# Performance work log

Measured on AMD Instinct MI355X. Metric: run time of the kernel, lower is better.

Reference implementation:

```python
import jax, jax.numpy as jnp
import numpy as np

H = 2048      # hidden_size
E = 16        # num_experts
I = 512       # moe_intermediate_size
IS = 2048     # shared_expert_intermediate_size
TOP_K = 2
B, S = 1, 2048


def setup_inputs() -> dict:
    key = jax.random.key(0)
    ks = jax.random.split(key, 9)
    std = 0.02
    return {
        "hidden_states": jax.random.normal(ks[0], (B, S, H), dtype=jnp.float32),
        "gate_w": jax.random.normal(ks[1], (E, H), dtype=jnp.float32) * std,
        "w1": jax.random.normal(ks[2], (E, I, H), dtype=jnp.float32) * std,  # gate_proj per expert
        "w2": jax.random.normal(ks[3], (E, H, I), dtype=jnp.float32) * std,  # down_proj per expert
        "w3": jax.random.normal(ks[4], (E, I, H), dtype=jnp.float32) * std,  # up_proj per expert
        "ws_gate": jax.random.normal(ks[5], (IS, H), dtype=jnp.float32) * std,  # shared gate_proj
        "ws_up": jax.random.normal(ks[6], (IS, H), dtype=jnp.float32) * std,    # shared up_proj
        "ws_down": jax.random.normal(ks[7], (H, IS), dtype=jnp.float32) * std,  # shared down_proj
        "shared_gate_w": jax.random.normal(ks[8], (1, H), dtype=jnp.float32) * std,
    }


def reference(hidden_states, gate_w, w1, w2, w3, ws_gate, ws_up, ws_down, shared_gate_w):
    b, s, h = hidden_states.shape
    x = hidden_states.reshape(-1, h)                     # [T, H]
    T = x.shape[0]

    # Router: softmax in fp32, top-k, renormalize (norm_topk_prob=True)
    router_logits = x @ gate_w.T                         # [T, E]
    routing = jax.nn.softmax(router_logits.astype(jnp.float32), axis=-1)
    topw, sel = jax.lax.top_k(routing, TOP_K)            # [T, K]
    topw = topw / jnp.sum(topw, axis=-1, keepdims=True)
    topw = topw.astype(x.dtype)

    # Scatter top-k weights into dense [T, E] combine matrix (torch_moe semantics)
    combine = jnp.zeros((T, E), dtype=x.dtype).at[jnp.arange(T)[:, None], sel].set(topw)

    # Expert SwiGLU MLPs evaluated densely, masked/weighted by combine
    hmid = jax.nn.silu(jnp.einsum('th,eih->tei', x, w1)) * jnp.einsum('th,eih->tei', x, w3)  # [T,E,I]
    hmid = hmid * combine[:, :, None]
    moe_out = jnp.einsum('tei,ehi->th', hmid, w2)        # [T, H]

    # Shared expert with sigmoid gate
    shared = (jax.nn.silu(x @ ws_gate.T) * (x @ ws_up.T)) @ ws_down.T  # [T, H]
    shared = jax.nn.sigmoid(x @ shared_gate_w.T) * shared

    return (moe_out + shared).reshape(b, s, h)
```

## Files before the change

### kernel.cpp

```cpp
#include <hip/hip_runtime.h>
#include <hip/hip_bf16.h>
#include <cmath>

#define HDIM 2048
#define NEXP 16
#define IDIM 512
#define ISDIM 2048
#define NTOK 2048
#define MAXT 48
#define ROWSCAP (MAXT * 128)

#define GU_EXP (MAXT * 4)
#define GU_SH ((NTOK / 128) * (ISDIM / 128))
#define DN_SH ((NTOK / 128) * (HDIM / 256))
#define DN_EXP (MAXT * 8)

typedef short bf16x8 __attribute__((ext_vector_type(8)));
typedef float f32x4 __attribute__((ext_vector_type(4)));
typedef unsigned short us;
typedef __attribute__((address_space(1))) const unsigned int* as1p;
typedef __attribute__((address_space(3))) unsigned int* as3p;

__device__ __forceinline__ us f2bf(float f) {
  unsigned int u = __builtin_bit_cast(unsigned int, f);
  u += 0x7FFFu + ((u >> 16) & 1u);
  return (us)(u >> 16);
}
__device__ __forceinline__ float bf2f(us v) {
  return __builtin_bit_cast(float, (unsigned)v << 16);
}

__device__ __forceinline__ void glds16(const void* g, void* l) {
  __builtin_amdgcn_global_load_lds((as1p)(unsigned long long)g,
                                   (as3p)(unsigned int)(unsigned long long)l, 16, 0, 0);
}

__device__ __forceinline__ void stage_cvt(const float* __restrict__ src,
                                          us* __restrict__ dst) {
  const float4* p = (const float4*)src;
  float4 a = p[0], b = p[1];
  unsigned u0 = __builtin_bit_cast(unsigned, a.x) + 0x8000u;
  unsigned u1 = __builtin_bit_cast(unsigned, a.y) + 0x8000u;
  unsigned u2 = __builtin_bit_cast(unsigned, a.z) + 0x8000u;
  unsigned u3 = __builtin_bit_cast(unsigned, a.w) + 0x8000u;
  unsigned u4 = __builtin_bit_cast(unsigned, b.x) + 0x8000u;
  unsigned u5 = __builtin_bit_cast(unsigned, b.y) + 0x8000u;
  unsigned u6 = __builtin_bit_cast(unsigned, b.z) + 0x8000u;
  unsigned u7 = __builtin_bit_cast(unsigned, b.w) + 0x8000u;
  int4 v;
  v.x = __builtin_amdgcn_perm(u1, u0, 0x07060302);
  v.y = __builtin_amdgcn_perm(u3, u2, 0x07060302);
  v.z = __builtin_amdgcn_perm(u5, u4, 0x07060302);
  v.w = __builtin_amdgcn_perm(u7, u6, 0x07060302);
  *(int4*)dst = v;
}

__global__ __launch_bounds__(256) void k_router(const float* __restrict__ x,
                                                const float* __restrict__ gate_w,
                                                const float* __restrict__ sgw,
                                                us* __restrict__ xb,
                                                int* __restrict__ sel,
                                                float* __restrict__ wnorm,
                                                float* __restrict__ sig,
                                                int* __restrict__ counts) {
  __shared__ float lg[4][17];
  int tid = threadIdx.x, wid = tid >> 6, lane = tid & 63;
  int t = blockIdx.x * 4 + wid;
  const float4* xrow = reinterpret_cast<const float4*>(x + (size_t)t * HDIM);
  float4 xv[8];
#pragma unroll
  for (int s = 0; s < 8; s++) xv[s] = xrow[s * 64 + lane];
  ushort4* xbrow = reinterpret_cast<ushort4*>(xb + (size_t)t * HDIM);
#pragma unroll
  for (int s = 0; s < 8; s++) {
    ushort4 o;
    o.x = f2bf(xv[s].x); o.y = f2bf(xv[s].y); o.z = f2bf(xv[s].z); o.w = f2bf(xv[s].w);
    xbrow[s * 64 + lane] = o;
  }
#pragma unroll 1
  for (int e = 0; e < 17; e++) {
    const float4* gr =
        reinterpret_cast<const float4*>(e < 16 ? gate_w + (size_t)e * HDIM : sgw);
    float acc = 0.f;
#pragma unroll
    for (int s = 0; s < 8; s++) {
      float4 g = gr[s * 64 + lane];
      acc += xv[s].x * g.x + xv[s].y * g.y + xv[s].z * g.z + xv[s].w * g.w;
    }
#pragma unroll
    for (int off = 32; off; off >>= 1) acc += __shfl_xor(acc, off, 64);
    if (lane == 0) lg[wid][e] = acc;
  }
  if (lane == 0) {
    float* L = lg[wid];
    int i1 = 0; float v1 = L[0];
    for (int i = 1; i < NEXP; i++) if (L[i] > v1) { v1 = L[i]; i1 = i; }
    int i2 = (i1 == 0) ? 1 : 0; float v2 = L[i2];
    for (int i = 0; i < NEXP; i++)
      if (i != i1 && i != i2 && L[i] > v2) { v2 = L[i]; i2 = i; }
    float wa = 1.f / (1.f + expf(v2 - v1));
    sel[2 * t] = i1; sel[2 * t + 1] = i2;
    wnorm[2 * t] = wa; wnorm[2 * t + 1] = 1.f - wa;
    sig[t] = 1.f / (1.f + expf(-L[16]));
    atomicAdd(&counts[i1], 1);
    atomicAdd(&counts[i2], 1);
  }
}

__global__ __launch_bounds__(256) void k_scan_scatter(const int* __restrict__ counts,
                                                      const int* __restrict__ sel,
                                                      const float* __restrict__ wnorm,
                                                      int* __restrict__ tile_expert,
                                                      int* __restrict__ row_token,
                                                      int* __restrict__ rowk,
                                                      float* __restrict__ rw) {
  __shared__ int offs_s[NEXP];
  __shared__ int fill_s[NEXP];
  int tid = threadIdx.x;
  for (int r = tid; r < ROWSCAP; r += 256) row_token[r] = -1;
  if (tid < NEXP) fill_s[tid] = 0;
  if (tid == 0) {
    int acc = 0;
    for (int e = 0; e < NEXP; e++) {
      offs_s[e] = acc;
      int nt = (counts[e] + 127) >> 7;
      for (int i = 0; i < nt; i++) tile_expert[(acc >> 7) + i] = e;
      acc += nt << 7;
    }
    for (int m = acc >> 7; m < MAXT; m++) tile_expert[m] = -1;
  }
  __syncthreads();
  for (int t = tid; t < NTOK; t += 256) {
    for (int k = 0; k < 2; k++) {
      int e = sel[2 * t + k];
      int pos = atomicAdd(&fill_s[e], 1);
      int row = offs_s[e] + pos;
      row_token[row] = t;
      rowk[row] = k;
      rw[row] = wnorm[2 * t + k];
    }
  }
}

__global__ __launch_bounds__(512) void k_gu(
    const us* __restrict__ xb, const float* __restrict__ w1,
    const float* __restrict__ w3, const float* __restrict__ wsg,
    const float* __restrict__ wsu, const int* __restrict__ tile_expert,
    const int* __restrict__ row_token, us* __restrict__ hmid,
    us* __restrict__ hs) {
  __shared__ us As[128 * 64];
  __shared__ us Bs[2][128 * 64];
  __shared__ int toks_s[128];
  int bid = blockIdx.x, tid = threadIdx.x;
  int w = tid >> 6, lane = tid & 63;
  const float *bG, *bU;
  us* outp;
  int mt, n0, ostride;
  if (bid < GU_EXP) {
    mt = bid >> 2; int nt = bid & 3;
    int e = tile_expert[mt];
    if (e < 0) return;
    if (tid < 128) {
      int tk = row_token[mt * 128 + tid];
      toks_s[tid] = tk < 0 ? 0 : tk;
    }
    bG = w1 + ((size_t)e * IDIM + nt * 128) * HDIM;
    bU = w3 + ((size_t)e * IDIM + nt * 128) * HDIM;
    outp = hmid; ostride = IDIM; n0 = nt * 128;
  } else {
    int sb = bid - GU_EXP;
    mt = sb >> 4; int nt = sb & 15;
    if (tid < 128) toks_s[tid] = mt * 128 + tid;
    bG = wsg + (size_t)(nt * 128) * HDIM;
    bU = wsu + (size_t)(nt * 128) * HDIM;
    outp = hs; ostride = ISDIM; n0 = nt * 128;
  }
  __syncthreads();
  int lr = lane >> 3, lc = lane & 7;
  int swz = (lc ^ lr) * 8;
  const us* aSrc0 = xb + (size_t)toks_s[w * 16 + lr] * HDIM + swz;
  const us* aSrc1 = xb + (size_t)toks_s[w * 16 + 8 + lr] * HDIM + swz;
  int r0 = tid >> 3, p0 = tid & 7, g0 = p0 ^ (r0 & 7);
  int r1 = (tid + 512) >> 3, g1 = p0 ^ (r1 & 7);
  size_t bo0 = (size_t)r0 * HDIM + g0 * 8;
  size_t bo1 = (size_t)r1 * HDIM + g1 * 8;
  int mat = w >> 2, sub = w & 3, wm = sub >> 1, wn = sub & 1;
  int quad = lane >> 4, l16 = lane & 15, sw = l16 & 7;
  f32x4 acc[4][4] = {};
  for (int k0 = 0; k0 < HDIM; k0 += 64) {
    glds16(aSrc0 + k0, As + w * 1024);
    glds16(aSrc1 + k0, As + w * 1024 + 512);
    stage_cvt(bG + bo0 + k0, &Bs[0][(r0 * 8 + p0) * 8]);
    stage_cvt(bG + bo1 + k0, &Bs[0][(r1 * 8 + p0) * 8]);
    stage_cvt(bU + bo0 + k0, &Bs[1][(r0 * 8 + p0) * 8]);
    stage_cvt(bU + bo1 + k0, &Bs[1][(r1 * 8 + p0) * 8]);
    __syncthreads();
#pragma unroll
    for (int ks = 0; ks < 2; ks++) {
      int cb = (ks * 4 + quad) ^ sw;
      bf16x8 af[4], bf[4];
#pragma unroll
      for (int ms = 0; ms < 4; ms++)
        af[ms] = *(const bf16x8*)&As[((wm * 64 + ms * 16 + l16) * 8 + cb) * 8];
#pragma unroll
      for (int ns = 0; ns < 4; ns++)
        bf[ns] = *(const bf16x8*)&Bs[mat][((wn * 64 + ns * 16 + l16) * 8 + cb) * 8];
#pragma unroll
      for (int ms = 0; ms < 4; ms++)
#pragma unroll
        for (int ns = 0; ns < 4; ns++)
          acc[ms][ns] = __builtin_amdgcn_mfma_f32_16x16x32_bf16(af[ms], bf[ns], acc[ms][ns], 0, 0, 0);
    }
    __syncthreads();
  }
  us* ub = (us*)Bs;
  if (mat == 1) {
#pragma unroll
    for (int ms = 0; ms < 4; ms++)
#pragma unroll
      for (int ns = 0; ns < 4; ns++)
#pragma unroll
        for (int r = 0; r < 4; r++) {
          int row = wm * 64 + ms * 16 + quad * 4 + r;
          int col = wn * 64 + ns * 16 + l16;
          ub[row * 128 + col] = f2bf(acc[ms][ns][r]);
        }
  }
  __syncthreads();
  if (mat == 0) {
#pragma unroll
    for (int ms = 0; ms < 4; ms++)
#pragma unroll
      for (int ns = 0; ns < 4; ns++)
#pragma unroll
        for (int r = 0; r < 4; r++) {
          int row = wm * 64 + ms * 16 + quad * 4 + r;
          int col = wn * 64 + ns * 16 + l16;
          float g = acc[ms][ns][r];
          float u = bf2f(ub[row * 128 + col]);
          float hv = (g / (1.f + __expf(-g))) * u;
          outp[(size_t)(mt * 128 + row) * ostride + n0 + col] = f2bf(hv);
        }
  }
}

__global__ __launch_bounds__(512) void k_down(
    const us* __restrict__ hmid, const us* __restrict__ hs,
    const float* __restrict__ w2, const float* __restrict__ wsd,
    const int* __restrict__ tile_expert, const int* __restrict__ row_token,
    const int* __restrict__ rowk, const float* __restrict__ rw,
    const float* __restrict__ sig, us* __restrict__ slab) {
  __shared__ us As[128 * 64];
  __shared__ us Bs[256 * 64];
  __shared__ int idx_s[128];
  __shared__ float wgt_s[128];
  int bid = blockIdx.x, tid = threadIdx.x;
  int w = tid >> 6, lane = tid & 63;
  const us* aBase;
  const float* bBase;
  int K, mt, n0;
  if (bid < DN_SH) {
    mt = bid >> 3; int nt = bid & 7;
    aBase = hs + (size_t)mt * 128 * ISDIM; K = ISDIM;
    bBase = wsd + (size_t)(nt * 256) * ISDIM;
    n0 = nt * 256;
    if (tid < 128) {
      int t = mt * 128 + tid;
      idx_s[tid] = 2 * NTOK * HDIM + t * HDIM;
      wgt_s[tid] = sig[t];
    }
  } else {
    int sb = bid - DN_SH;
    mt = sb >> 3; int nt = sb & 7;
    int e = tile_expert[mt];
    if (e < 0) return;
    aBase = hmid + (size_t)mt * 128 * IDIM; K = IDIM;
    bBase = w2 + ((size_t)e * HDIM + nt * 256) * IDIM;
    n0 = nt * 256;
    if (tid < 128) {
      int tk = row_token[mt * 128 + tid];
      if (tk < 0) { idx_s[tid] = -1; wgt_s[tid] = 0.f; }
      else {
        idx_s[tid] = (rowk[mt * 128 + tid] * NTOK + tk) * HDIM;
        wgt_s[tid] = rw[mt * 128 + tid];
      }
    }
  }
  __syncthreads();
  int lr = lane >> 3, lc = lane & 7;
  int swz = (lc ^ lr) * 8;
  const us* aSrc0 = aBase + (size_t)(w * 16 + lr) * K + swz;
  const us* aSrc1 = aBase + (size_t)(w * 16 + 8 + lr) * K + swz;
  int r0 = tid >> 3, p0 = tid & 7;
  int wmn = w >> 2, wn = w & 3;
  int quad = lane >> 4, l16 = lane & 15, sw = l16 & 7;
  f32x4 acc[4][4] = {};
  for (int k0 = 0; k0 < K; k0 += 64) {
    glds16(aSrc0 + k0, As + w * 1024);
    glds16(aSrc1 + k0, As + w * 1024 + 512);
#pragma unroll
    for (int j = 0; j < 4; j++) {
      int row = r0 + j * 64;
      int gc = p0 ^ (row & 7);
      stage_cvt(bBase + (size_t)row * K + gc * 8 + k0, &Bs[(row * 8 + p0) * 8]);
    }
    __syncthreads();
#pragma unroll
    for (int ks = 0; ks < 2; ks++) {
      int cb = (ks * 4 + quad) ^ sw;
      bf16x8 af[4], bf[4];
#pragma unroll
      for (int ms = 0; ms < 4; ms++)
        af[ms] = *(const bf16x8*)&As[((wmn * 64 + ms * 16 + l16) * 8 + cb) * 8];
#pragma unroll
      for (int ns = 0; ns < 4; ns++)
        bf[ns] = *(const bf16x8*)&Bs[((wn * 64 + ns * 16 + l16) * 8 + cb) * 8];
#pragma unroll
      for (int ms = 0; ms < 4; ms++)
#pragma unroll
        for (int ns = 0; ns < 4; ns++)
          acc[ms][ns] = __builtin_amdgcn_mfma_f32_16x16x32_bf16(af[ms], bf[ns], acc[ms][ns], 0, 0, 0);
    }
    __syncthreads();
  }
#pragma unroll
  for (int ms = 0; ms < 4; ms++)
#pragma unroll
    for (int r = 0; r < 4; r++) {
      int rr = wmn * 64 + ms * 16 + quad * 4 + r;
      int ix = idx_s[rr];
      if (ix >= 0) {
        float wgt = wgt_s[rr];
        us* orow = slab + (size_t)ix + n0 + wn * 64;
#pragma unroll
        for (int ns = 0; ns < 4; ns++)
          orow[ns * 16 + l16] = f2bf(wgt * acc[ms][ns][r]);
      }
    }
}

__global__ __launch_bounds__(256) void k_combine(const us* __restrict__ slab,
                                                 float* __restrict__ out) {
  size_t i = ((size_t)blockIdx.x * 256 + threadIdx.x) * 8;
  bf16x8 a = *(const bf16x8*)(slab + i);
  bf16x8 b = *(const bf16x8*)(slab + (size_t)NTOK * HDIM + i);
  bf16x8 c = *(const bf16x8*)(slab + 2 * (size_t)NTOK * HDIM + i);
  float4 o[2];
#pragma unroll
  for (int j = 0; j < 8; j++)
    ((float*)o)[j] = bf2f((us)a[j]) + bf2f((us)b[j]) + bf2f((us)c[j]);
  *(float4*)(out + i) = o[0];
  *(float4*)(out + i + 4) = o[1];
}

extern "C" void kernel_launch(void* const* d_in, const int* in_sizes, int n_in,
                              void* d_out, int out_size, void* d_ws, size_t ws_size,
                              hipStream_t stream) {
  const float* x = (const float*)d_in[0];
  const float* gate_w = (const float*)d_in[1];
  const float* w1 = (const float*)d_in[2];
  const float* w2 = (const float*)d_in[3];
  const float* w3 = (const float*)d_in[4];
  const float* wsg = (const float*)d_in[5];
  const float* wsu = (const float*)d_in[6];
  const float* wsd = (const float*)d_in[7];
  const float* sgw = (const float*)d_in[8];
  float* out = (float*)d_out;

  us* xb = (us*)d_ws;
  us* hs = xb + (size_t)NTOK * HDIM;
  us* hmid = hs + (size_t)NTOK * ISDIM;
  us* slab = hmid + (size_t)ROWSCAP * IDIM;
  float* rw = (float*)(slab + (size_t)3 * NTOK * HDIM);
  float* wnorm = rw + ROWSCAP;
  float* sig = wnorm + 2 * NTOK;
  int* sel = (int*)(sig + NTOK);
  int* row_token = sel + 2 * NTOK;
  int* rowk = row_token + ROWSCAP;
  int* counts = rowk + ROWSCAP;
  int* tile_expert = counts + NEXP;

  hipMemsetAsync(counts, 0, NEXP * sizeof(int), stream);
  k_router<<<dim3(NTOK / 4), dim3(256), 0, stream>>>(x, gate_w, sgw, xb, sel, wnorm,
                                                     sig, counts);
  k_scan_scatter<<<dim3(1), dim3(256), 0, stream>>>(counts, sel, wnorm, tile_expert,
                                                    row_token, rowk, rw);
  k_gu<<<dim3(GU_EXP + GU_SH), dim3(512), 0, stream>>>(
      xb, w1, w3, wsg, wsu, tile_expert, row_token, hmid, hs);
  k_down<<<dim3(DN_SH + DN_EXP), dim3(512), 0, stream>>>(
      hmid, hs, w2, wsd, tile_expert, row_token, rowk, rw, sig, slab);
  k_combine<<<dim3(NTOK * HDIM / 2048), dim3(256), 0, stream>>>(slab, out);
}
```

Baseline: 459.5 us.

## Pre-convert weights to bf16 and load GEMM B tiles via direct LDS loads

Adds a kernel that converts all expert and shared weight matrices from fp32 to bf16 into workspace each call. The gate/up and down GEMMs then stage the B operand with asynchronous global-to-LDS loads of bf16 instead of loading fp32 into registers and converting. This halves the bytes of repeated weight tile reads and removes conversion work from the GEMM inner loop, at the cost of an extra full pass reading and writing all weights.

```diff
diff --git a/kernel.cpp b/kernel.cpp
--- a/kernel.cpp
+++ b/kernel.cpp
@@ -1,5 +1,4 @@
 #include <hip/hip_runtime.h>
-#include <hip/hip_bf16.h>
 #include <cmath>
 
 #define HDIM 2048
@@ -53,6 +52,25 @@
   v.z = __builtin_amdgcn_perm(u5, u4, 0x07060302);
   v.w = __builtin_amdgcn_perm(u7, u6, 0x07060302);
   *(int4*)dst = v;
+}
+
+__global__ __launch_bounds__(256) void k_cvt(
+    const float* __restrict__ w1, const float* __restrict__ w2,
+    const float* __restrict__ w3, const float* __restrict__ wsg,
+    const float* __restrict__ wsu, const float* __restrict__ wsd,
+    us* __restrict__ w1b, us* __restrict__ w2b, us* __restrict__ w3b,
+    us* __restrict__ wsgb, us* __restrict__ wsub, us* __restrict__ wsdb) {
+  int b = blockIdx.x;
+  const float* src;
+  us* dst;
+  if (b < 8192) { src = w1; dst = w1b; }
+  else if (b < 16384) { src = w2; dst = w2b; b -= 8192; }
+  else if (b < 24576) { src = w3; dst = w3b; b -= 16384; }
+  else if (b < 26624) { src = wsg; dst = wsgb; b -= 24576; }
+  else if (b < 28672) { src = wsu; dst = wsub; b -= 26624; }
+  else { src = wsd; dst = wsdb; b -= 28672; }
+  size_t off = ((size_t)b * 256 + threadIdx.x) * 8;
+  stage_cvt(src + off, dst + off);
 }
 
 __global__ __launch_bounds__(256) void k_router(const float* __restrict__ x,
@@ -143,9 +161,9 @@
 }
 
 __global__ __launch_bounds__(512) void k_gu(
-    const us* __restrict__ xb, const float* __restrict__ w1,
-    const float* __restrict__ w3, const float* __restrict__ wsg,
-    const float* __restrict__ wsu, const int* __restrict__ tile_expert,
+    const us* __restrict__ xb, const us* __restrict__ w1b,
+    const us* __restrict__ w3b, const us* __restrict__ wsgb,
+    const us* __restrict__ wsub, const int* __restrict__ tile_expert,
     const int* __restrict__ row_token, us* __restrict__ hmid,
     us* __restrict__ hs) {
   __shared__ us As[128 * 64];
@@ -153,7 +171,7 @@
   __shared__ int toks_s[128];
   int bid = blockIdx.x, tid = threadIdx.x;
   int w = tid >> 6, lane = tid & 63;
-  const float *bG, *bU;
+  const us *bG, *bU;
   us* outp;
   int mt, n0, ostride;
   if (bid < GU_EXP) {
@@ -164,15 +182,15 @@
       int tk = row_token[mt * 128 + tid];
       toks_s[tid] = tk < 0 ? 0 : tk;
     }
-    bG = w1 + ((size_t)e * IDIM + nt * 128) * HDIM;
-    bU = w3 + ((size_t)e * IDIM + nt * 128) * HDIM;
+    bG = w1b + ((size_t)e * IDIM + nt * 128) * HDIM;
+    bU = w3b + ((size_t)e * IDIM + nt * 128) * HDIM;
     outp = hmid; ostride = IDIM; n0 = nt * 128;
   } else {
     int sb = bid - GU_EXP;
     mt = sb >> 4; int nt = sb & 15;
     if (tid < 128) toks_s[tid] = mt * 128 + tid;
-    bG = wsg + (size_t)(nt * 128) * HDIM;
-    bU = wsu + (size_t)(nt * 128) * HDIM;
+    bG = wsgb + (size_t)(nt * 128) * HDIM;
+    bU = wsub + (size_t)(nt * 128) * HDIM;
     outp = hs; ostride = ISDIM; n0 = nt * 128;
   }
   __syncthreads();
@@ -180,20 +198,17 @@
   int swz = (lc ^ lr) * 8;
   const us* aSrc0 = xb + (size_t)toks_s[w * 16 + lr] * HDIM + swz;
   const us* aSrc1 = xb + (size_t)toks_s[w * 16 + 8 + lr] * HDIM + swz;
-  int r0 = tid >> 3, p0 = tid & 7, g0 = p0 ^ (r0 & 7);
-  int r1 = (tid + 512) >> 3, g1 = p0 ^ (r1 & 7);
-  size_t bo0 = (size_t)r0 * HDIM + g0 * 8;
-  size_t bo1 = (size_t)r1 * HDIM + g1 * 8;
   int mat = w >> 2, sub = w & 3, wm = sub >> 1, wn = sub & 1;
+  const us* bSrc = (mat ? bU : bG) + (size_t)(sub * 32 + lr) * HDIM + swz;
+  us* bDst = &Bs[mat][sub * 32 * 64];
   int quad = lane >> 4, l16 = lane & 15, sw = l16 & 7;
   f32x4 acc[4][4] = {};
   for (int k0 = 0; k0 < HDIM; k0 += 64) {
     glds16(aSrc0 + k0, As + w * 1024);
     glds16(aSrc1 + k0, As + w * 1024 + 512);
-    stage_cvt(bG + bo0 + k0, &Bs[0][(r0 * 8 + p0) * 8]);
-    stage_cvt(bG + bo1 + k0, &Bs[0][(r1 * 8 + p0) * 8]);
-    stage_cvt(bU + bo0 + k0, &Bs[1][(r0 * 8 + p0) * 8]);
-    stage_cvt(bU + bo1 + k0, &Bs[1][(r1 * 8 + p0) * 8]);
+#pragma unroll
+    for (int g = 0; g < 4; g++)
+      glds16(bSrc + (size_t)(g * 8) * HDIM + k0, bDst + g * 512);
     __syncthreads();
 #pragma unroll
     for (int ks = 0; ks < 2; ks++) {
@@ -246,7 +261,7 @@
 
 __global__ __launch_bounds__(512) void k_down(
     const us* __restrict__ hmid, const us* __restrict__ hs,
-    const float* __restrict__ w2, const float* __restrict__ wsd,
+    const us* __restrict__ w2b, const us* __restrict__ wsdb,
     const int* __restrict__ tile_expert, const int* __restrict__ row_token,
     const int* __restrict__ rowk, const float* __restrict__ rw,
     const float* __restrict__ sig, us* __restrict__ slab) {
@@ -257,12 +272,12 @@
   int bid = blockIdx.x, tid = threadIdx.x;
   int w = tid >> 6, lane = tid & 63;
   const us* aBase;
-  const float* bBase;
+  const us* bBase;
   int K, mt, n0;
   if (bid < DN_SH) {
     mt = bid >> 3; int nt = bid & 7;
     aBase = hs + (size_t)mt * 128 * ISDIM; K = ISDIM;
-    bBase = wsd + (size_t)(nt * 256) * ISDIM;
+    bBase = wsdb + (size_t)(nt * 256) * ISDIM;
     n0 = nt * 256;
     if (tid < 128) {
       int t = mt * 128 + tid;
@@ -275,7 +290,7 @@
     int e = tile_expert[mt];
     if (e < 0) return;
     aBase = hmid + (size_t)mt * 128 * IDIM; K = IDIM;
-    bBase = w2 + ((size_t)e * HDIM + nt * 256) * IDIM;
+    bBase = w2b + ((size_t)e * HDIM + nt * 256) * IDIM;
     n0 = nt * 256;
     if (tid < 128) {
       int tk = row_token[mt * 128 + tid];
@@ -291,7 +306,8 @@
   int swz = (lc ^ lr) * 8;
   const us* aSrc0 = aBase + (size_t)(w * 16 + lr) * K + swz;
   const us* aSrc1 = aBase + (size_t)(w * 16 + 8 + lr) * K + swz;
-  int r0 = tid >> 3, p0 = tid & 7;
+  const us* bSrc = bBase + (size_t)(w * 32 + lr) * K + swz;
+  us* bDst = Bs + w * 32 * 64;
   int wmn = w >> 2, wn = w & 3;
   int quad = lane >> 4, l16 = lane & 15, sw = l16 & 7;
   f32x4 acc[4][4] = {};
@@ -299,11 +315,8 @@
     glds16(aSrc0 + k0, As + w * 1024);
     glds16(aSrc1 + k0, As + w * 1024 + 512);
 #pragma unroll
-    for (int j = 0; j < 4; j++) {
-      int row = r0 + j * 64;
-      int gc = p0 ^ (row & 7);
-      stage_cvt(bBase + (size_t)row * K + gc * 8 + k0, &Bs[(row * 8 + p0) * 8]);
-    }
+    for (int g = 0; g < 4; g++)
+      glds16(bSrc + (size_t)(g * 8) * K + k0, bDst + g * 512);
     __syncthreads();
 #pragma unroll
     for (int ks = 0; ks < 2; ks++) {
@@ -371,7 +384,13 @@
   us* hs = xb + (size_t)NTOK * HDIM;
   us* hmid = hs + (size_t)NTOK * ISDIM;
   us* slab = hmid + (size_t)ROWSCAP * IDIM;
-  float* rw = (float*)(slab + (size_t)3 * NTOK * HDIM);
+  us* w1b = slab + (size_t)3 * NTOK * HDIM;
+  us* w3b = w1b + (size_t)NEXP * IDIM * HDIM;
+  us* w2b = w3b + (size_t)NEXP * IDIM * HDIM;
+  us* wsgb = w2b + (size_t)NEXP * HDIM * IDIM;
+  us* wsub = wsgb + (size_t)ISDIM * HDIM;
+  us* wsdb = wsub + (size_t)ISDIM * HDIM;
+  float* rw = (float*)(wsdb + (size_t)HDIM * ISDIM);
   float* wnorm = rw + ROWSCAP;
   float* sig = wnorm + 2 * NTOK;
   int* sel = (int*)(sig + NTOK);
@@ -381,13 +400,15 @@
   int* tile_expert = counts + NEXP;
 
   hipMemsetAsync(counts, 0, NEXP * sizeof(int), stream);
+  k_cvt<<<dim3(30720), dim3(256), 0, stream>>>(w1, w2, w3, wsg, wsu, wsd,
+                                               w1b, w2b, w3b, wsgb, wsub, wsdb);
   k_router<<<dim3(NTOK / 4), dim3(256), 0, stream>>>(x, gate_w, sgw, xb, sel, wnorm,
                                                      sig, counts);
   k_scan_scatter<<<dim3(1), dim3(256), 0, stream>>>(counts, sel, wnorm, tile_expert,
                                                     row_token, rowk, rw);
   k_gu<<<dim3(GU_EXP + GU_SH), dim3(512), 0, stream>>>(
-      xb, w1, w3, wsg, wsu, tile_expert, row_token, hmid, hs);
+      xb, w1b, w3b, wsgb, wsub, tile_expert, row_token, hmid, hs);
   k_down<<<dim3(DN_SH + DN_EXP), dim3(512), 0, stream>>>(
-      hmid, hs, w2, wsd, tile_expert, row_token, rowk, rw, sig, slab);
+      hmid, hs, w2b, wsdb, tile_expert, row_token, rowk, rw, sig, slab);
   k_combine<<<dim3(NTOK * HDIM / 2048), dim3(256), 0, stream>>>(slab, out);
 }
```

After: 464.0 us. Within noise of the previous version (+1.0%).

## Software-pipeline weight and activation loads in gate-up and down GEMM kernels

Applied to the files above, without the earlier changes.

Both GEMM kernels now double-buffer the activation LDS tile and prefetch the next k-step's fp32 weights into registers while the current tile runs its MFMA work. The aim is to hide global-memory latency behind compute instead of serializing load, convert and compute each iteration. The cost is more registers and LDS, which may lower occupancy. The trailing syncthreads is replaced by a raw s_barrier fenced with sched_barriers, which relies on the next iteration's barrier to order the async LDS loads.

```diff
diff --git a/kernel.cpp b/kernel.cpp
--- a/kernel.cpp
+++ b/kernel.cpp
@@ -1,5 +1,4 @@
 #include <hip/hip_runtime.h>
-#include <hip/hip_bf16.h>
 #include <cmath>
 
 #define HDIM 2048
@@ -35,10 +34,14 @@
                                    (as3p)(unsigned int)(unsigned long long)l, 16, 0, 0);
 }
 
-__device__ __forceinline__ void stage_cvt(const float* __restrict__ src,
-                                          us* __restrict__ dst) {
+__device__ __forceinline__ void load8(const float* __restrict__ src,
+                                      float4& a, float4& b) {
   const float4* p = (const float4*)src;
-  float4 a = p[0], b = p[1];
+  a = p[0];
+  b = p[1];
+}
+
+__device__ __forceinline__ void cvt8_store(float4 a, float4 b, us* __restrict__ dst) {
   unsigned u0 = __builtin_bit_cast(unsigned, a.x) + 0x8000u;
   unsigned u1 = __builtin_bit_cast(unsigned, a.y) + 0x8000u;
   unsigned u2 = __builtin_bit_cast(unsigned, a.z) + 0x8000u;
@@ -148,7 +151,7 @@
     const float* __restrict__ wsu, const int* __restrict__ tile_expert,
     const int* __restrict__ row_token, us* __restrict__ hmid,
     us* __restrict__ hs) {
-  __shared__ us As[128 * 64];
+  __shared__ us As[2][128 * 64];
   __shared__ us Bs[2][128 * 64];
   __shared__ int toks_s[128];
   int bid = blockIdx.x, tid = threadIdx.x;
@@ -181,27 +184,42 @@
   const us* aSrc0 = xb + (size_t)toks_s[w * 16 + lr] * HDIM + swz;
   const us* aSrc1 = xb + (size_t)toks_s[w * 16 + 8 + lr] * HDIM + swz;
   int r0 = tid >> 3, p0 = tid & 7, g0 = p0 ^ (r0 & 7);
-  int r1 = (tid + 512) >> 3, g1 = p0 ^ (r1 & 7);
+  int r1 = r0 + 64, g1 = p0 ^ (r1 & 7);
   size_t bo0 = (size_t)r0 * HDIM + g0 * 8;
   size_t bo1 = (size_t)r1 * HDIM + g1 * 8;
   int mat = w >> 2, sub = w & 3, wm = sub >> 1, wn = sub & 1;
   int quad = lane >> 4, l16 = lane & 15, sw = l16 & 7;
+  us* aCur = As[0];
+  us* aNxt = As[1];
+  glds16(aSrc0, aCur + w * 1024);
+  glds16(aSrc1, aCur + w * 1024 + 512);
+  float4 g0a, g0b, g1a, g1b, u0a, u0b, u1a, u1b;
+  load8(bG + bo0, g0a, g0b);
+  load8(bG + bo1, g1a, g1b);
+  load8(bU + bo0, u0a, u0b);
+  load8(bU + bo1, u1a, u1b);
   f32x4 acc[4][4] = {};
   for (int k0 = 0; k0 < HDIM; k0 += 64) {
-    glds16(aSrc0 + k0, As + w * 1024);
-    glds16(aSrc1 + k0, As + w * 1024 + 512);
-    stage_cvt(bG + bo0 + k0, &Bs[0][(r0 * 8 + p0) * 8]);
-    stage_cvt(bG + bo1 + k0, &Bs[0][(r1 * 8 + p0) * 8]);
-    stage_cvt(bU + bo0 + k0, &Bs[1][(r0 * 8 + p0) * 8]);
-    stage_cvt(bU + bo1 + k0, &Bs[1][(r1 * 8 + p0) * 8]);
+    cvt8_store(g0a, g0b, &Bs[0][(r0 * 8 + p0) * 8]);
+    cvt8_store(g1a, g1b, &Bs[0][(r1 * 8 + p0) * 8]);
+    cvt8_store(u0a, u0b, &Bs[1][(r0 * 8 + p0) * 8]);
+    cvt8_store(u1a, u1b, &Bs[1][(r1 * 8 + p0) * 8]);
     __syncthreads();
+    if (k0 + 64 < HDIM) {
+      glds16(aSrc0 + k0 + 64, aNxt + w * 1024);
+      glds16(aSrc1 + k0 + 64, aNxt + w * 1024 + 512);
+      load8(bG + bo0 + k0 + 64, g0a, g0b);
+      load8(bG + bo1 + k0 + 64, g1a, g1b);
+      load8(bU + bo0 + k0 + 64, u0a, u0b);
+      load8(bU + bo1 + k0 + 64, u1a, u1b);
+    }
 #pragma unroll
     for (int ks = 0; ks < 2; ks++) {
       int cb = (ks * 4 + quad) ^ sw;
       bf16x8 af[4], bf[4];
 #pragma unroll
       for (int ms = 0; ms < 4; ms++)
-        af[ms] = *(const bf16x8*)&As[((wm * 64 + ms * 16 + l16) * 8 + cb) * 8];
+        af[ms] = *(const bf16x8*)&aCur[((wm * 64 + ms * 16 + l16) * 8 + cb) * 8];
 #pragma unroll
       for (int ns = 0; ns < 4; ns++)
         bf[ns] = *(const bf16x8*)&Bs[mat][((wn * 64 + ns * 16 + l16) * 8 + cb) * 8];
@@ -211,7 +229,10 @@
         for (int ns = 0; ns < 4; ns++)
           acc[ms][ns] = __builtin_amdgcn_mfma_f32_16x16x32_bf16(af[ms], bf[ns], acc[ms][ns], 0, 0, 0);
     }
-    __syncthreads();
+    __builtin_amdgcn_sched_barrier(0);
+    __builtin_amdgcn_s_barrier();
+    __builtin_amdgcn_sched_barrier(0);
+    us* t = aCur; aCur = aNxt; aNxt = t;
   }
   us* ub = (us*)Bs;
   if (mat == 1) {
@@ -250,7 +271,7 @@
     const int* __restrict__ tile_expert, const int* __restrict__ row_token,
     const int* __restrict__ rowk, const float* __restrict__ rw,
     const float* __restrict__ sig, us* __restrict__ slab) {
-  __shared__ us As[128 * 64];
+  __shared__ us As[2][128 * 64];
   __shared__ us Bs[256 * 64];
   __shared__ int idx_s[128];
   __shared__ float wgt_s[128];
@@ -291,27 +312,41 @@
   int swz = (lc ^ lr) * 8;
   const us* aSrc0 = aBase + (size_t)(w * 16 + lr) * K + swz;
   const us* aSrc1 = aBase + (size_t)(w * 16 + 8 + lr) * K + swz;
-  int r0 = tid >> 3, p0 = tid & 7;
+  int r0 = tid >> 3, p0 = tid & 7, gc = p0 ^ (r0 & 7);
+  const float* bS = bBase + (size_t)r0 * K + gc * 8;
   int wmn = w >> 2, wn = w & 3;
   int quad = lane >> 4, l16 = lane & 15, sw = l16 & 7;
+  us* aCur = As[0];
+  us* aNxt = As[1];
+  glds16(aSrc0, aCur + w * 1024);
+  glds16(aSrc1, aCur + w * 1024 + 512);
+  float4 b0a, b0b, b1a, b1b, b2a, b2b, b3a, b3b;
+  load8(bS + (size_t)0 * 64 * K, b0a, b0b);
+  load8(bS + (size_t)1 * 64 * K, b1a, b1b);
+  load8(bS + (size_t)2 * 64 * K, b2a, b2b);
+  load8(bS + (size_t)3 * 64 * K, b3a, b3b);
   f32x4 acc[4][4] = {};
   for (int k0 = 0; k0 < K; k0 += 64) {
-    glds16(aSrc0 + k0, As + w * 1024);
-    glds16(aSrc1 + k0, As + w * 1024 + 512);
-#pragma unroll
-    for (int j = 0; j < 4; j++) {
-      int row = r0 + j * 64;
-      int gc = p0 ^ (row & 7);
-      stage_cvt(bBase + (size_t)row * K + gc * 8 + k0, &Bs[(row * 8 + p0) * 8]);
-    }
+    cvt8_store(b0a, b0b, &Bs[((r0 + 0) * 8 + p0) * 8]);
+    cvt8_store(b1a, b1b, &Bs[((r0 + 64) * 8 + p0) * 8]);
+    cvt8_store(b2a, b2b, &Bs[((r0 + 128) * 8 + p0) * 8]);
+    cvt8_store(b3a, b3b, &Bs[((r0 + 192) * 8 + p0) * 8]);
     __syncthreads();
+    if (k0 + 64 < K) {
+      glds16(aSrc0 + k0 + 64, aNxt + w * 1024);
+      glds16(aSrc1 + k0 + 64, aNxt + w * 1024 + 512);
+      load8(bS + (size_t)0 * 64 * K + k0 + 64, b0a, b0b);
+      load8(bS + (size_t)1 * 64 * K + k0 + 64, b1a, b1b);
+      load8(bS + (size_t)2 * 64 * K + k0 + 64, b2a, b2b);
+      load8(bS + (size_t)3 * 64 * K + k0 + 64, b3a, b3b);
+    }
 #pragma unroll
     for (int ks = 0; ks < 2; ks++) {
       int cb = (ks * 4 + quad) ^ sw;
       bf16x8 af[4], bf[4];
 #pragma unroll
       for (int ms = 0; ms < 4; ms++)
-        af[ms] = *(const bf16x8*)&As[((wmn * 64 + ms * 16 + l16) * 8 + cb) * 8];
+        af[ms] = *(const bf16x8*)&aCur[((wmn * 64 + ms * 16 + l16) * 8 + cb) * 8];
 #pragma unroll
       for (int ns = 0; ns < 4; ns++)
         bf[ns] = *(const bf16x8*)&Bs[((wn * 64 + ns * 16 + l16) * 8 + cb) * 8];
@@ -321,7 +356,10 @@
         for (int ns = 0; ns < 4; ns++)
           acc[ms][ns] = __builtin_amdgcn_mfma_f32_16x16x32_bf16(af[ms], bf[ns], acc[ms][ns], 0, 0, 0);
     }
-    __syncthreads();
+    __builtin_amdgcn_sched_barrier(0);
+    __builtin_amdgcn_s_barrier();
+    __builtin_amdgcn_sched_barrier(0);
+    us* t = aCur; aCur = aNxt; aNxt = t;
   }
 #pragma unroll
   for (int ms = 0; ms < 4; ms++)
```

Result: no change. 466.4 us (+1.5%).
